# Kernel optimization log

Measured on AMD Instinct MI355X. Metric: run time of the kernel, lower is better.

The kernel has to match this reference:

```python
import jax, jax.numpy as jnp
import numpy as np

N = 524288
ENC_POS, ENC_DIR, HID, N_LAYERS, SKIP = 63, 27, 256, 8, 4


def _linear_params(key, in_dim, out_dim):
    kw, _ = jax.random.split(key)
    bound = float(np.sqrt(6.0 / in_dim))  # kaiming-uniform-ish
    W = jax.random.uniform(kw, (out_dim, in_dim), jnp.float32, -bound, bound)
    b = jnp.zeros((out_dim,), jnp.float32)
    return W, b


def setup_inputs() -> dict:
    key = jax.random.key(0)
    keys = jax.random.split(key, N_LAYERS + 6)
    inp = {
        "enc_pos": jax.random.normal(keys[0], (N, ENC_POS), jnp.float32),
        "enc_dir": jax.random.normal(keys[1], (N, ENC_DIR), jnp.float32),
    }
    in_dim = ENC_POS
    for i in range(N_LAYERS):
        d_in = in_dim + ENC_POS if i == SKIP else in_dim
        W, b = _linear_params(keys[2 + i], d_in, HID)
        inp[f"W{i}"], inp[f"b{i}"] = W, b
        in_dim = HID
    inp["Wf"], inp["bf"] = _linear_params(keys[-4], HID, HID)
    inp["Ws"], inp["bs"] = _linear_params(keys[-3], HID, 1)
    inp["Wc1"], inp["bc1"] = _linear_params(keys[-2], HID + ENC_DIR, HID // 2)
    inp["Wc2"], inp["bc2"] = _linear_params(keys[-1], HID // 2, 3)
    return inp


def reference(enc_pos, enc_dir,
              W0, b0, W1, b1, W2, b2, W3, b3, W4, b4, W5, b5, W6, b6, W7, b7,
              Wf, bf, Ws, bs, Wc1, bc1, Wc2, bc2):
    Ws_mlp = [(W0, b0), (W1, b1), (W2, b2), (W3, b3),
              (W4, b4), (W5, b5), (W6, b6), (W7, b7)]
    h = enc_pos
    for i, (W, b) in enumerate(Ws_mlp):
        if i == SKIP:
            h = jnp.concatenate([h, enc_pos], axis=-1)  # [N, 256+63]
        h = jax.nn.relu(h @ W.T + b)
    sigma_raw = h @ Ws.T + bs            # [N, 1]
    feature = h @ Wf.T + bf              # [N, 256]
    color_in = jnp.concatenate([feature, enc_dir], axis=-1)
    color_hidden = jax.nn.relu(color_in @ Wc1.T + bc1)
    color_raw = color_hidden @ Wc2.T + bc2  # [N, 3]
    return jnp.concatenate([color_raw, sigma_raw], axis=-1)  # [N, 4]
```

## Files before the change

kernel.cpp:

```cpp
#include <hip/hip_runtime.h>
#include <hip/hip_bf16.h>

typedef __attribute__((ext_vector_type(8))) short bf16x8;
typedef __attribute__((ext_vector_type(4))) float f32x4;
typedef __attribute__((ext_vector_type(2))) unsigned int u32x2;

#define MFMA_BF16(a, b, c) __builtin_amdgcn_mfma_f32_16x16x32_bf16((a), (b), (c), 0, 0, 0)

static __device__ __forceinline__ unsigned short f2bf(float f) {
  unsigned int u = __builtin_bit_cast(unsigned int, f);
  u += 0x7FFF + ((u >> 16) & 1);
  return (unsigned short)(u >> 16);
}
static __device__ __forceinline__ unsigned int pk2(float a, float b) {
  return (unsigned int)f2bf(a) | ((unsigned int)f2bf(b) << 16);
}

enum : int {
  OFF_W0  = 0,
  OFF_W1  = 16384,
  OFF_W2  = 81920,
  OFF_W3  = 147456,
  OFF_W4  = 212992,
  OFF_W5  = 294912,
  OFF_W6  = 360448,
  OFF_W7  = 425984,
  OFF_WF  = 491520,
  OFF_WC1 = 557056,
  OFF_WS  = 593920,
  OFF_WC2 = 598016,
  W_TOTAL = 600064
};

struct Seg { const float* src; int rows_src, kin, nb, ks, off; };
struct SegArgs { Seg s[12]; };

__global__ void convert_weights(SegArgs args, unsigned short* __restrict__ dst) {
  int idx = blockIdx.x * 256 + threadIdx.x;
  #pragma unroll
  for (int i = 0; i < 12; i++) {
    const Seg sg = args.s[i];
    const int sz = sg.nb * sg.ks * 512;
    if (idx < sz) {
      const int f = idx >> 9, rm = idx & 511;
      const int lane = rm >> 3, j = rm & 7;
      const int ks = f / sg.nb, nb = f - ks * sg.nb;
      const int n = nb * 16 + (lane & 15);
      const int k = ks * 32 + ((lane >> 4) << 3) + j;
      float v = (n < sg.rows_src && k < sg.kin) ? sg.src[n * sg.kin + k] : 0.0f;
      dst[sg.off + idx] = f2bf(v);
      return;
    }
    idx -= sz;
  }
}


template<int WF, int HF>
static __device__ __forceinline__ void zero_acc(f32x4 (&acc)[WF][HF]) {
  #pragma unroll
  for (int wf = 0; wf < WF; wf++)
    #pragma unroll
    for (int hf = 0; hf < HF; hf++)
      acc[wf][hf] = (f32x4){0.f, 0.f, 0.f, 0.f};
}

template<int WF, int HF>
static __device__ __forceinline__ void init_bias(
    f32x4 (&acc)[WF][HF], const float* __restrict__ bias, int colBase) {
  const int lq4 = ((threadIdx.x & 63) >> 4) * 4;
  #pragma unroll
  for (int wf = 0; wf < WF; wf++) {
    const f32x4 b = *(const f32x4*)(bias + colBase + wf * 16 + lq4);
    #pragma unroll
    for (int hf = 0; hf < HF; hf++) acc[wf][hf] = b;
  }
}

template<int WF, int HF, int KS, int NB, int ASTRIDE>
static __device__ __forceinline__ void gemm_frag(
    f32x4 (&acc)[WF][HF],
    const unsigned short* __restrict__ wseg, int nbBase, int ksOff,
    const unsigned short* __restrict__ aLds, int rowBase)
{
  const int lane = threadIdx.x & 63;
  const int lr   = lane & 15;
  const int lq8  = (lane >> 4) * 8;
  #pragma unroll 2
  for (int ks = 0; ks < KS; ks++) {
    bf16x8 w[WF], h[HF];
    #pragma unroll
    for (int wf = 0; wf < WF; wf++)
      w[wf] = *(const bf16x8*)(wseg + (((ksOff + ks) * NB + nbBase + wf) << 9) + lane * 8);
    #pragma unroll
    for (int hf = 0; hf < HF; hf++) {
      const int row = rowBase + hf * 16 + lr;
      const int col = ks * 32 + lq8;
      h[hf] = *(const bf16x8*)((const char*)aLds +
                (((row * ASTRIDE + col) << 1) ^ ((row & 7) << 4)));
    }
    #pragma unroll
    for (int wf = 0; wf < WF; wf++)
      #pragma unroll
      for (int hf = 0; hf < HF; hf++)
        acc[wf][hf] = MFMA_BF16(w[wf], h[hf], acc[wf][hf]);
  }
}

template<int WF, int HF, bool RELU, int ASTRIDE>
static __device__ __forceinline__ void store_act(
    const f32x4 (&acc)[WF][HF], int colBase, unsigned short* __restrict__ lds)
{
  const int lane = threadIdx.x & 63;
  const int lr   = lane & 15;
  const int lq4  = (lane >> 4) * 4;
  #pragma unroll
  for (int wf = 0; wf < WF; wf++) {
    const int col = colBase + wf * 16 + lq4;
    #pragma unroll
    for (int hf = 0; hf < HF; hf++) {
      const int row = hf * 16 + lr;
      f32x4 v = acc[wf][hf];
      if (RELU) {
        v[0] = fmaxf(v[0], 0.f); v[1] = fmaxf(v[1], 0.f);
        v[2] = fmaxf(v[2], 0.f); v[3] = fmaxf(v[3], 0.f);
      }
      u32x2 p; p[0] = pk2(v[0], v[1]); p[1] = pk2(v[2], v[3]);
      *(u32x2*)((char*)lds +
          (((row * ASTRIDE + col) << 1) ^ ((row & 7) << 4))) = p;
    }
  }
}

__global__ __launch_bounds__(256, 2) void nerf_main(
    const float* __restrict__ enc_pos, const float* __restrict__ enc_dir,
    const unsigned short* __restrict__ Wt,
    const float* __restrict__ b0, const float* __restrict__ b1,
    const float* __restrict__ b2, const float* __restrict__ b3,
    const float* __restrict__ b4, const float* __restrict__ b5,
    const float* __restrict__ b6, const float* __restrict__ b7,
    const float* __restrict__ bfb, const float* __restrict__ bsb,
    const float* __restrict__ bc1, const float* __restrict__ bc2,
    float* __restrict__ out)
{
  __shared__ __align__(16) unsigned short act[128 * 256];
  __shared__ __align__(16) unsigned short posb[128 * 64];

  const int tid  = threadIdx.x;
  const int wave = tid >> 6;
  const int lane = tid & 63;
  const int lr   = lane & 15;
  const int lq   = lane >> 4;
  const int row0 = blockIdx.x * 128;

  for (int i = tid; i < 128 * 64; i += 256) {
    const int r = i >> 6, c = i & 63;
    const float v = (c < 63) ? enc_pos[(size_t)(row0 + r) * 63 + c] : 0.0f;
    *(unsigned short*)((char*)posb + (((r * 64 + c) << 1) ^ ((r & 7) << 4))) = f2bf(v);
  }
  __syncthreads();

  f32x4 acc[4][8];

  init_bias<4, 8>(acc, b0, wave * 64);
  gemm_frag<4, 8, 2, 16, 64>(acc, Wt + OFF_W0, wave * 4, 0, posb, 0);
  store_act<4, 8, true, 256>(acc, wave * 64, act);
  __syncthreads();
  init_bias<4, 8>(acc, b1, wave * 64);
  gemm_frag<4, 8, 8, 16, 256>(acc, Wt + OFF_W1, wave * 4, 0, act, 0);
  __syncthreads();
  store_act<4, 8, true, 256>(acc, wave * 64, act);
  __syncthreads();
  init_bias<4, 8>(acc, b2, wave * 64);
  gemm_frag<4, 8, 8, 16, 256>(acc, Wt + OFF_W2, wave * 4, 0, act, 0);
  __syncthreads();
  store_act<4, 8, true, 256>(acc, wave * 64, act);
  __syncthreads();
  init_bias<4, 8>(acc, b3, wave * 64);
  gemm_frag<4, 8, 8, 16, 256>(acc, Wt + OFF_W3, wave * 4, 0, act, 0);
  __syncthreads();
  store_act<4, 8, true, 256>(acc, wave * 64, act);
  __syncthreads();
  init_bias<4, 8>(acc, b4, wave * 64);
  gemm_frag<4, 8, 8, 16, 256>(acc, Wt + OFF_W4, wave * 4, 0, act, 0);
  gemm_frag<4, 8, 2, 16, 64>(acc, Wt + OFF_W4, wave * 4, 8, posb, 0);
  __syncthreads();
  store_act<4, 8, true, 256>(acc, wave * 64, act);
  __syncthreads();
  init_bias<4, 8>(acc, b5, wave * 64);
  gemm_frag<4, 8, 8, 16, 256>(acc, Wt + OFF_W5, wave * 4, 0, act, 0);
  __syncthreads();
  store_act<4, 8, true, 256>(acc, wave * 64, act);
  __syncthreads();
  init_bias<4, 8>(acc, b6, wave * 64);
  gemm_frag<4, 8, 8, 16, 256>(acc, Wt + OFF_W6, wave * 4, 0, act, 0);
  __syncthreads();
  store_act<4, 8, true, 256>(acc, wave * 64, act);
  __syncthreads();
  init_bias<4, 8>(acc, b7, wave * 64);
  gemm_frag<4, 8, 8, 16, 256>(acc, Wt + OFF_W7, wave * 4, 0, act, 0);
  __syncthreads();
  store_act<4, 8, true, 256>(acc, wave * 64, act);
  __syncthreads();

  for (int i = tid; i < 128 * 32; i += 256) {
    const int r = i >> 5, c = i & 31;
    const float v = (c < 27) ? enc_dir[(size_t)(row0 + r) * 27 + c] : 0.0f;
    *(unsigned short*)((char*)posb + (((r * 64 + c) << 1) ^ ((r & 7) << 4))) = f2bf(v);
  }

  f32x4 sacc[1][2];
  zero_acc(sacc);
  gemm_frag<1, 2, 8, 1, 256>(sacc, Wt + OFF_WS, 0, 0, act, wave * 32);

  init_bias<4, 8>(acc, bfb, wave * 64);
  gemm_frag<4, 8, 8, 16, 256>(acc, Wt + OFF_WF, wave * 4, 0, act, 0);
  __syncthreads();
  store_act<4, 8, false, 256>(acc, wave * 64, act);
  if (lq == 0) {
    const float bv = bsb[0];
    #pragma unroll
    for (int hf = 0; hf < 2; hf++)
      out[(size_t)(row0 + wave * 32 + hf * 16 + lr) * 4 + 3] = sacc[0][hf][0] + bv;
  }
  __syncthreads();

  {
    f32x4 cacc[2][8];
    init_bias<2, 8>(cacc, bc1, wave * 32);
    gemm_frag<2, 8, 8, 8, 256>(cacc, Wt + OFF_WC1, wave * 2, 0, act, 0);
    gemm_frag<2, 8, 1, 8, 64>(cacc, Wt + OFF_WC1, wave * 2, 8, posb, 0);
    __syncthreads();
    store_act<2, 8, true, 256>(cacc, wave * 32, act);
    __syncthreads();
  }

  {
    f32x4 c2[1][2];
    zero_acc(c2);
    gemm_frag<1, 2, 4, 1, 256>(c2, Wt + OFF_WC2, 0, 0, act, wave * 32);
    if (lq == 0) {
      #pragma unroll
      for (int hf = 0; hf < 2; hf++) {
        const size_t row = row0 + wave * 32 + hf * 16 + lr;
        #pragma unroll
        for (int r = 0; r < 3; r++)
          out[row * 4 + r] = c2[0][hf][r] + bc2[r];
      }
    }
  }
}

extern "C" void kernel_launch(void* const* d_in, const int* in_sizes, int n_in,
                              void* d_out, int out_size, void* d_ws, size_t ws_size,
                              hipStream_t stream) {
  const float* enc_pos = (const float*)d_in[0];
  const float* enc_dir = (const float*)d_in[1];
  unsigned short* wbf  = (unsigned short*)d_ws;

  SegArgs sa;
  sa.s[0]  = { (const float*)d_in[2],  256, 63,  16, 2,  OFF_W0  };
  sa.s[1]  = { (const float*)d_in[4],  256, 256, 16, 8,  OFF_W1  };
  sa.s[2]  = { (const float*)d_in[6],  256, 256, 16, 8,  OFF_W2  };
  sa.s[3]  = { (const float*)d_in[8],  256, 256, 16, 8,  OFF_W3  };
  sa.s[4]  = { (const float*)d_in[10], 256, 319, 16, 10, OFF_W4  };
  sa.s[5]  = { (const float*)d_in[12], 256, 256, 16, 8,  OFF_W5  };
  sa.s[6]  = { (const float*)d_in[14], 256, 256, 16, 8,  OFF_W6  };
  sa.s[7]  = { (const float*)d_in[16], 256, 256, 16, 8,  OFF_W7  };
  sa.s[8]  = { (const float*)d_in[18], 256, 256, 16, 8,  OFF_WF  };
  sa.s[9]  = { (const float*)d_in[22], 128, 283, 8,  9,  OFF_WC1 };
  sa.s[10] = { (const float*)d_in[20], 1,   256, 1,  8,  OFF_WS  };
  sa.s[11] = { (const float*)d_in[24], 3,   128, 1,  4,  OFF_WC2 };

  convert_weights<<<W_TOTAL / 256, 256, 0, stream>>>(sa, wbf);

  const int N = in_sizes[0] / 63;
  const int blocks = N / 128;
  nerf_main<<<blocks, 256, 0, stream>>>(
      enc_pos, enc_dir, wbf,
      (const float*)d_in[3],  (const float*)d_in[5],
      (const float*)d_in[7],  (const float*)d_in[9],
      (const float*)d_in[11], (const float*)d_in[13],
      (const float*)d_in[15], (const float*)d_in[17],
      (const float*)d_in[19], (const float*)d_in[21],
      (const float*)d_in[23], (const float*)d_in[25],
      (float*)d_out);
}
```

Baseline: 736.8 us.

## Replace XOR-swizzled LDS layout with padded rows and use hardware bf16 pack

Switches the shared-memory activation and encoding buffers from an XOR-swizzled layout to padded row strides (264 and 72 elements), which simplifies address arithmetic in the GEMM inner loop and in stores. It also fully unrolls the K loop with incremented weight pointers, and replaces the software round-to-nearest bf16 conversion with the v_cvt_pk_bf16_f32 instruction. The aim is to cut VALU address and conversion overhead around the MFMAs. In exchange LDS use grows a little, which could affect occupancy at two blocks per CU, and full unrolling raises register pressure.

```diff
diff --git a/kernel.cpp b/kernel.cpp
--- a/kernel.cpp
+++ b/kernel.cpp
@@ -12,8 +12,10 @@
   u += 0x7FFF + ((u >> 16) & 1);
   return (unsigned short)(u >> 16);
 }
-static __device__ __forceinline__ unsigned int pk2(float a, float b) {
-  return (unsigned int)f2bf(a) | ((unsigned int)f2bf(b) << 16);
+static __device__ __forceinline__ unsigned int cvtpk(float lo, float hi) {
+  unsigned int r;
+  asm("v_cvt_pk_bf16_f32 %0, %1, %2" : "=v"(r) : "v"(lo), "v"(hi));
+  return r;
 }
 
 enum : int {
@@ -86,24 +88,23 @@
   const int lane = threadIdx.x & 63;
   const int lr   = lane & 15;
   const int lq8  = (lane >> 4) * 8;
-  #pragma unroll 2
+  const unsigned short* wp = wseg + ((ksOff * NB + nbBase) << 9) + lane * 8;
+  const unsigned short* ap = aLds + (rowBase + lr) * ASTRIDE + lq8;
+  #pragma unroll
   for (int ks = 0; ks < KS; ks++) {
     bf16x8 w[WF], h[HF];
     #pragma unroll
     for (int wf = 0; wf < WF; wf++)
-      w[wf] = *(const bf16x8*)(wseg + (((ksOff + ks) * NB + nbBase + wf) << 9) + lane * 8);
-    #pragma unroll
-    for (int hf = 0; hf < HF; hf++) {
-      const int row = rowBase + hf * 16 + lr;
-      const int col = ks * 32 + lq8;
-      h[hf] = *(const bf16x8*)((const char*)aLds +
-                (((row * ASTRIDE + col) << 1) ^ ((row & 7) << 4)));
-    }
+      w[wf] = *(const bf16x8*)(wp + (wf << 9));
+    #pragma unroll
+    for (int hf = 0; hf < HF; hf++)
+      h[hf] = *(const bf16x8*)(ap + hf * 16 * ASTRIDE + ks * 32);
     #pragma unroll
     for (int wf = 0; wf < WF; wf++)
       #pragma unroll
       for (int hf = 0; hf < HF; hf++)
         acc[wf][hf] = MFMA_BF16(w[wf], h[hf], acc[wf][hf]);
+    wp += (NB << 9);
   }
 }
 
@@ -125,9 +126,8 @@
         v[0] = fmaxf(v[0], 0.f); v[1] = fmaxf(v[1], 0.f);
         v[2] = fmaxf(v[2], 0.f); v[3] = fmaxf(v[3], 0.f);
       }
-      u32x2 p; p[0] = pk2(v[0], v[1]); p[1] = pk2(v[2], v[3]);
-      *(u32x2*)((char*)lds +
-          (((row * ASTRIDE + col) << 1) ^ ((row & 7) << 4))) = p;
+      u32x2 p; p[0] = cvtpk(v[0], v[1]); p[1] = cvtpk(v[2], v[3]);
+      *(u32x2*)(lds + row * ASTRIDE + col) = p;
     }
   }
 }
@@ -143,8 +143,8 @@
     const float* __restrict__ bc1, const float* __restrict__ bc2,
     float* __restrict__ out)
 {
-  __shared__ __align__(16) unsigned short act[128 * 256];
-  __shared__ __align__(16) unsigned short posb[128 * 64];
+  __shared__ __align__(16) unsigned short act[128 * 264];
+  __shared__ __align__(16) unsigned short posb[128 * 72];
 
   const int tid  = threadIdx.x;
   const int wave = tid >> 6;
@@ -156,67 +156,67 @@
   for (int i = tid; i < 128 * 64; i += 256) {
     const int r = i >> 6, c = i & 63;
     const float v = (c < 63) ? enc_pos[(size_t)(row0 + r) * 63 + c] : 0.0f;
-    *(unsigned short*)((char*)posb + (((r * 64 + c) << 1) ^ ((r & 7) << 4))) = f2bf(v);
+    posb[r * 72 + c] = f2bf(v);
   }
   __syncthreads();
 
   f32x4 acc[4][8];
 
   init_bias<4, 8>(acc, b0, wave * 64);
-  gemm_frag<4, 8, 2, 16, 64>(acc, Wt + OFF_W0, wave * 4, 0, posb, 0);
-  store_act<4, 8, true, 256>(acc, wave * 64, act);
+  gemm_frag<4, 8, 2, 16, 72>(acc, Wt + OFF_W0, wave * 4, 0, posb, 0);
+  store_act<4, 8, true, 264>(acc, wave * 64, act);
   __syncthreads();
   init_bias<4, 8>(acc, b1, wave * 64);
-  gemm_frag<4, 8, 8, 16, 256>(acc, Wt + OFF_W1, wave * 4, 0, act, 0);
-  __syncthreads();
-  store_act<4, 8, true, 256>(acc, wave * 64, act);
+  gemm_frag<4, 8, 8, 16, 264>(acc, Wt + OFF_W1, wave * 4, 0, act, 0);
+  __syncthreads();
+  store_act<4, 8, true, 264>(acc, wave * 64, act);
   __syncthreads();
   init_bias<4, 8>(acc, b2, wave * 64);
-  gemm_frag<4, 8, 8, 16, 256>(acc, Wt + OFF_W2, wave * 4, 0, act, 0);
-  __syncthreads();
-  store_act<4, 8, true, 256>(acc, wave * 64, act);
+  gemm_frag<4, 8, 8, 16, 264>(acc, Wt + OFF_W2, wave * 4, 0, act, 0);
+  __syncthreads();
+  store_act<4, 8, true, 264>(acc, wave * 64, act);
   __syncthreads();
   init_bias<4, 8>(acc, b3, wave * 64);
-  gemm_frag<4, 8, 8, 16, 256>(acc, Wt + OFF_W3, wave * 4, 0, act, 0);
-  __syncthreads();
-  store_act<4, 8, true, 256>(acc, wave * 64, act);
+  gemm_frag<4, 8, 8, 16, 264>(acc, Wt + OFF_W3, wave * 4, 0, act, 0);
+  __syncthreads();
+  store_act<4, 8, true, 264>(acc, wave * 64, act);
   __syncthreads();
   init_bias<4, 8>(acc, b4, wave * 64);
-  gemm_frag<4, 8, 8, 16, 256>(acc, Wt + OFF_W4, wave * 4, 0, act, 0);
-  gemm_frag<4, 8, 2, 16, 64>(acc, Wt + OFF_W4, wave * 4, 8, posb, 0);
-  __syncthreads();
-  store_act<4, 8, true, 256>(acc, wave * 64, act);
+  gemm_frag<4, 8, 8, 16, 264>(acc, Wt + OFF_W4, wave * 4, 0, act, 0);
+  gemm_frag<4, 8, 2, 16, 72>(acc, Wt + OFF_W4, wave * 4, 8, posb, 0);
+  __syncthreads();
+  store_act<4, 8, true, 264>(acc, wave * 64, act);
   __syncthreads();
   init_bias<4, 8>(acc, b5, wave * 64);
-  gemm_frag<4, 8, 8, 16, 256>(acc, Wt + OFF_W5, wave * 4, 0, act, 0);
-  __syncthreads();
-  store_act<4, 8, true, 256>(acc, wave * 64, act);
+  gemm_frag<4, 8, 8, 16, 264>(acc, Wt + OFF_W5, wave * 4, 0, act, 0);
+  __syncthreads();
+  store_act<4, 8, true, 264>(acc, wave * 64, act);
   __syncthreads();
   init_bias<4, 8>(acc, b6, wave * 64);
-  gemm_frag<4, 8, 8, 16, 256>(acc, Wt + OFF_W6, wave * 4, 0, act, 0);
-  __syncthreads();
-  store_act<4, 8, true, 256>(acc, wave * 64, act);
+  gemm_frag<4, 8, 8, 16, 264>(acc, Wt + OFF_W6, wave * 4, 0, act, 0);
+  __syncthreads();
+  store_act<4, 8, true, 264>(acc, wave * 64, act);
   __syncthreads();
   init_bias<4, 8>(acc, b7, wave * 64);
-  gemm_frag<4, 8, 8, 16, 256>(acc, Wt + OFF_W7, wave * 4, 0, act, 0);
-  __syncthreads();
-  store_act<4, 8, true, 256>(acc, wave * 64, act);
+  gemm_frag<4, 8, 8, 16, 264>(acc, Wt + OFF_W7, wave * 4, 0, act, 0);
+  __syncthreads();
+  store_act<4, 8, true, 264>(acc, wave * 64, act);
   __syncthreads();
 
   for (int i = tid; i < 128 * 32; i += 256) {
     const int r = i >> 5, c = i & 31;
     const float v = (c < 27) ? enc_dir[(size_t)(row0 + r) * 27 + c] : 0.0f;
-    *(unsigned short*)((char*)posb + (((r * 64 + c) << 1) ^ ((r & 7) << 4))) = f2bf(v);
+    posb[r * 72 + c] = f2bf(v);
   }
 
   f32x4 sacc[1][2];
   zero_acc(sacc);
-  gemm_frag<1, 2, 8, 1, 256>(sacc, Wt + OFF_WS, 0, 0, act, wave * 32);
+  gemm_frag<1, 2, 8, 1, 264>(sacc, Wt + OFF_WS, 0, 0, act, wave * 32);
 
   init_bias<4, 8>(acc, bfb, wave * 64);
-  gemm_frag<4, 8, 8, 16, 256>(acc, Wt + OFF_WF, wave * 4, 0, act, 0);
-  __syncthreads();
-  store_act<4, 8, false, 256>(acc, wave * 64, act);
+  gemm_frag<4, 8, 8, 16, 264>(acc, Wt + OFF_WF, wave * 4, 0, act, 0);
+  __syncthreads();
+  store_act<4, 8, false, 264>(acc, wave * 64, act);
   if (lq == 0) {
     const float bv = bsb[0];
     #pragma unroll
@@ -228,17 +228,17 @@
   {
     f32x4 cacc[2][8];
     init_bias<2, 8>(cacc, bc1, wave * 32);
-    gemm_frag<2, 8, 8, 8, 256>(cacc, Wt + OFF_WC1, wave * 2, 0, act, 0);
-    gemm_frag<2, 8, 1, 8, 64>(cacc, Wt + OFF_WC1, wave * 2, 8, posb, 0);
+    gemm_frag<2, 8, 8, 8, 264>(cacc, Wt + OFF_WC1, wave * 2, 0, act, 0);
+    gemm_frag<2, 8, 1, 8, 72>(cacc, Wt + OFF_WC1, wave * 2, 8, posb, 0);
     __syncthreads();
-    store_act<2, 8, true, 256>(cacc, wave * 32, act);
+    store_act<2, 8, true, 264>(cacc, wave * 32, act);
     __syncthreads();
   }
 
   {
     f32x4 c2[1][2];
     zero_acc(c2);
-    gemm_frag<1, 2, 4, 1, 256>(c2, Wt + OFF_WC2, 0, 0, act, wave * 32);
+    gemm_frag<1, 2, 4, 1, 264>(c2, Wt + OFF_WC2, 0, 0, act, wave * 32);
     if (lq == 0) {
       #pragma unroll
       for (int hf = 0; hf < 2; hf++) {
```

After: 809.8 us, median of 2. 1.1x slower.
